# Kernel tuning notes

Measured on AMD Instinct MI355X. Metric: run time of the kernel, lower is better.

The kernel has to match this reference:

```python
import jax, jax.numpy as jnp
import numpy as np

N = 100000      # nodes
E = 1600000     # edges (before self loops)
M = 40          # n_markers
HID = 128       # hidden
HEADS = 4
DH = HID // HEADS  # 32 per-head dim
LAT = 64
NEG_SLOPE = 0.2
EPS = 1e-5


def setup_inputs() -> dict:
    key = jax.random.key(0)
    ks = jax.random.split(key, 20)
    r = lambda k, shape, s=0.05: (jax.random.normal(k, shape, jnp.float32) * s)
    x = jax.random.normal(ks[0], (N, M), jnp.float32)
    edge_index = jax.random.randint(ks[1], (2, E), 0, N, jnp.int64)
    return {
        "x": x,
        "edge_index": edge_index,
        "Wp": r(ks[2], (M, HID)), "bp": jnp.zeros((HID,), jnp.float32),
        "W1l": r(ks[3], (HID, HID)), "W1r": r(ks[4], (HID, HID)),
        "att1": r(ks[5], (HEADS, DH)), "b1": jnp.zeros((HID,), jnp.float32),
        "W2l": r(ks[6], (HID, HID)), "W2r": r(ks[7], (HID, HID)),
        "att2": r(ks[8], (HEADS, DH)), "b2": jnp.zeros((HID,), jnp.float32),
        "g1": jnp.ones((HID,), jnp.float32), "be1": jnp.zeros((HID,), jnp.float32),
        "g2": jnp.ones((HID,), jnp.float32), "be2": jnp.zeros((HID,), jnp.float32),
        "Wo": r(ks[9], (HID, LAT)), "bo": jnp.zeros((LAT,), jnp.float32),
    }


def _layernorm(z, g, b):
    mu = jnp.mean(z, axis=-1, keepdims=True)
    var = jnp.mean(jnp.square(z - mu), axis=-1, keepdims=True)
    return (z - mu) * jax.lax.rsqrt(var + EPS) * g + b


def _gatv2(h, src, dst, Wl, Wr, att, bias):
    # h: [N, HID]; per-head source/target projections (GATv2, share_weights=False)
    hl = (h @ Wl).reshape(N, HEADS, DH)  # messages (source side)
    hr = (h @ Wr).reshape(N, HEADS, DH)  # target side
    # per-edge attention logits: a^T LeakyReLU(hl[src] + hr[dst])
    e = jax.nn.leaky_relu(hl[src] + hr[dst], NEG_SLOPE)      # [Etot, HEADS, DH]
    logits = jnp.einsum('ehd,hd->eh', e, att)                # [Etot, HEADS]
    # segment softmax over edges sharing the same destination node
    m = jax.ops.segment_max(logits, dst, num_segments=N)     # [N, HEADS]
    ex = jnp.exp(logits - m[dst])
    denom = jax.ops.segment_sum(ex, dst, num_segments=N)     # [N, HEADS]
    alpha = ex / denom[dst]                                  # [Etot, HEADS]
    # scatter-aggregate weighted source messages
    out = jax.ops.segment_sum(hl[src] * alpha[:, :, None], dst, num_segments=N)
    return out.reshape(N, HID) + bias


def reference(x, edge_index, Wp, bp, W1l, W1r, att1, b1, W2l, W2r, att2, b2,
              g1, be1, g2, be2, Wo, bo):
    loops = jnp.arange(N, dtype=edge_index.dtype)
    src = jnp.concatenate([edge_index[0], loops])  # PyG adds self loops by default
    dst = jnp.concatenate([edge_index[1], loops])
    h = x @ Wp + bp
    h = _layernorm(jax.nn.gelu(_gatv2(h, src, dst, W1l, W1r, att1, b1), approximate=False) + h, g1, be1)
    h = _layernorm(jax.nn.gelu(_gatv2(h, src, dst, W2l, W2r, att2, b2), approximate=False) + h, g2, be2)
    return h @ Wo + bo
```

## Files before the change

### kernel.cpp

```cpp
#include <hip/hip_runtime.h>
#include <hip/hip_bf16.h>
#include <math.h>

#define NN   100000
#define EE   1600000
#define ETOT 1700000
#define MM   40
#define HID  128
#define LAT  64
#define NB   391
#define CHUNK 4096

typedef unsigned short u16;
typedef unsigned int   u32;
typedef unsigned long long u64;

typedef __attribute__((ext_vector_type(8))) short bf16x8;
typedef __attribute__((ext_vector_type(4))) float f32x4;
typedef __attribute__((ext_vector_type(2))) float f32x2;

__device__ __forceinline__ float bf2f(u16 a) {
    return __uint_as_float(((u32)a) << 16);
}
__device__ __forceinline__ u16 f2bf(float f) {
    u32 u = __float_as_uint(f);
    u32 r = (u + 0x7fffu + ((u >> 16) & 1u)) >> 16;
    return (u16)r;
}
__device__ __forceinline__ f32x2 unpk(u32 u) {
    f32x2 r;
    r.x = __uint_as_float(u << 16);
    r.y = __uint_as_float(u & 0xffff0000u);
    return r;
}
__device__ __forceinline__ float exp2_hw(float x) {
    float d;
    asm("v_exp_f32 %0, %1" : "=v"(d) : "v"(x));
    return d;
}
__device__ __forceinline__ void gload_lds16(const void* g, void* l) {
    __builtin_amdgcn_global_load_lds(
        (const __attribute__((address_space(1))) void*)g,
        (__attribute__((address_space(3))) void*)l, 16, 0, 0);
}
__device__ __forceinline__ float gelu_t(float x) {
    float x2 = x * x;
    float y = x * fmaf(0.0713548162726f, x2, 1.59576912161f);
    return x / (1.f + __expf(-y));
}

#define Vbp   0
#define Vatt1 128
#define Vb1   256
#define Vg1   384
#define Vbe1  512
#define Vatt2 640
#define Vb2   768
#define Vg2   896
#define Vbe2  1024
#define Vbo   1152
#define VTOT  1216

#define BWp   0
#define BW1l  8192
#define BW1r  24576
#define BW2l  40960
#define BW2r  57344
#define BWo   73728
#define BTOT  90112

#define NXB   15625
#define NVB   5
#define NWB   352

__device__ __forceinline__ int sniff_bf_wave(const u32* __restrict__ x_raw) {
    int lane = threadIdx.x & 63;
    u32 w = x_raw[lane];
    u16 lo = (u16)(w & 0xffffu);
    int e = (lo >> 7) & 0xFF;
    int ok = (e >= 118 && e <= 133) ? 1 : 0;
    u64 b = __ballot(ok);
    return (__popcll(b) >= 48) ? 1 : 0;
}

__device__ __forceinline__ void edge_decode(const int* __restrict__ ei, int is64, int e,
                                            int& src, int& dst) {
    if (e < EE) {
        src = is64 ? ei[2 * e] : ei[e];
        int idx = EE + e;
        dst = is64 ? ei[2 * idx] : ei[idx];
    } else {
        src = e - EE; dst = src;
    }
}

__global__ __launch_bounds__(256) void prep_kernel(
    const void* __restrict__ x, const u32* __restrict__ ei_raw,
    const void* p0, const void* p1, const void* p2, const void* p3, const void* p4,
    const void* p5, const void* p6, const void* p7, const void* p8, const void* p9,
    const void* w0, const void* w1, const void* w2, const void* w3, const void* w4,
    const void* w5,
    u16* __restrict__ xb, float* __restrict__ wv, u16* __restrict__ wbf,
    int* __restrict__ flags, u32* __restrict__ gbucket, u32* __restrict__ dcnt,
    u32* __restrict__ gcur, u32* __restrict__ dcur)
{
    const u32* x_raw = (const u32*)x;
    int isbf = sniff_bf_wave(x_raw);
    int t = threadIdx.x;
    int b = blockIdx.x;

    if (b == 0) {
        if (t < 64) {
            u32 a = ei_raw[2 * t + 1] | ei_raw[129 + 2 * t];
            u64 nz = __ballot(a != 0u);
            if (t == 0) { flags[0] = (nz == 0uLL) ? 1 : 0; flags[1] = isbf; }
        }
        gbucket[t] = 0; gbucket[t + 256] = 0;
        gcur[t] = 0;    gcur[t + 256] = 0;
        if (t < 64) { dcnt[t] = 0; dcur[t] = 0; }
        return;
    }
    if (b <= NXB) {
        int i = (b - 1) * 256 + t;
        xb[i] = isbf ? ((const u16*)x)[i] : f2bf(((const float*)x)[i]);
        return;
    }
    if (b <= NXB + NVB) {
        int i = (b - 1 - NXB) * 256 + t;
        if (i >= VTOT) return;
        const int offs[11] = {Vbp, Vatt1, Vb1, Vg1, Vbe1, Vatt2, Vb2, Vg2, Vbe2, Vbo, VTOT};
        const void* ps[10] = {p0,p1,p2,p3,p4,p5,p6,p7,p8,p9};
        int s = 0;
#pragma unroll
        for (int k = 1; k < 10; k++) s += (i >= offs[k]) ? 1 : 0;
        int j = i - offs[s];
        const void* p = ps[s];
        wv[i] = isbf ? bf2f(((const u16*)p)[j]) : ((const float*)p)[j];
        return;
    }
    {
        int i = (b - 1 - NXB - NVB) * 256 + t;
        const int offs[7] = {BWp, BW1l, BW1r, BW2l, BW2r, BWo, BTOT};
        const int Ks[6]   = {40, 128, 128, 128, 128, 128};
        const int Ncs[6]  = {128, 128, 128, 128, 128, 64};
        const int Kps[6]  = {64, 128, 128, 128, 128, 128};
        const void* ps[6] = {w0,w1,w2,w3,w4,w5};
        int s = 0;
#pragma unroll
        for (int k = 1; k < 6; k++) s += (i >= offs[k]) ? 1 : 0;
        int j = i - offs[s];
        int Kp = Kps[s];
        int n = j / Kp, k = j % Kp;
        u16 v = 0;
        if (k < Ks[s] && n < Ncs[s]) {
            const void* p = ps[s];
            int src = k * Ncs[s] + n;
            v = isbf ? ((const u16*)p)[src] : f2bf(((const float*)p)[src]);
        }
        wbf[i] = v;
    }
}

__global__ __launch_bounds__(256) void bucket_hist_kernel(
    const int* __restrict__ ei, const int* __restrict__ flags, u32* __restrict__ gbucket)
{
    __shared__ u32 h[512];
    int t = threadIdx.x;
    h[t] = 0; h[t + 256] = 0;
    __syncthreads();
    int is64 = flags[0];
    int base = blockIdx.x * CHUNK;
#pragma unroll
    for (int j = 0; j < CHUNK / 256; j++) {
        int e = base + j * 256 + t;
        if (e < ETOT) {
            int src, dst;
            edge_decode(ei, is64, e, src, dst);
            atomicAdd(&h[dst >> 8], 1u);
        }
    }
    __syncthreads();
    if (h[t])       atomicAdd(&gbucket[t], h[t]);
    if (h[t + 256]) atomicAdd(&gbucket[t + 256], h[t + 256]);
}

__global__ __launch_bounds__(256) void bin_pass_kernel(
    const int* __restrict__ ei, const int* __restrict__ flags,
    const u32* __restrict__ gbucket, u32* __restrict__ gcur, u64* __restrict__ pairs)
{
    __shared__ u32 bh[512];
    __shared__ u32 boff[512];
    __shared__ u32 bbs[512];
    __shared__ u32 bcur[512];
    __shared__ u32 bsc[512];
    __shared__ u64 stage[CHUNK];
    __shared__ u32 ts[256];

    int t = threadIdx.x;
    bh[t] = 0; bh[t + 256] = 0;
    __syncthreads();
    int is64 = flags[0];
    int base = blockIdx.x * CHUNK;
    int chunk_n = ETOT - base; if (chunk_n > CHUNK) chunk_n = CHUNK;

#pragma unroll
    for (int j = 0; j < CHUNK / 256; j++) {
        int e = base + j * 256 + t;
        if (e < ETOT) {
            int src, dst;
            edge_decode(ei, is64, e, src, dst);
            atomicAdd(&bh[dst >> 8], 1u);
        }
    }
    __syncthreads();

    {
        u32 g0v = (2 * t     < NB) ? gbucket[2 * t]     : 0;
        u32 g1v = (2 * t + 1 < NB) ? gbucket[2 * t + 1] : 0;
        u32 ps = g0v + g1v;
        ts[t] = ps; __syncthreads();
        for (int d = 1; d < 256; d <<= 1) {
            u32 v = (t >= d) ? ts[t - d] : 0;
            __syncthreads();
            ts[t] += v;
            __syncthreads();
        }
        u32 ex = ts[t] - ps;
        bsc[2 * t] = ex; bsc[2 * t + 1] = ex + g0v;
    }
    __syncthreads();

    u32 s0 = bh[2 * t], s1 = bh[2 * t + 1];
    u32 tsum = s0 + s1;
    ts[t] = tsum; __syncthreads();
    for (int d = 1; d < 256; d <<= 1) {
        u32 v = (t >= d) ? ts[t - d] : 0;
        __syncthreads();
        ts[t] += v;
        __syncthreads();
    }
    u32 excl = ts[t] - tsum;
    boff[2 * t] = excl; boff[2 * t + 1] = excl + s0;
    bcur[2 * t] = excl; bcur[2 * t + 1] = excl + s0;
    __syncthreads();
    if (t < NB && bh[t]) bbs[t] = bsc[t] + atomicAdd(&gcur[t], bh[t]);
    if (t + 256 < NB && bh[t + 256]) bbs[t + 256] = bsc[t + 256] + atomicAdd(&gcur[t + 256], bh[t + 256]);
    __syncthreads();
#pragma unroll
    for (int j = 0; j < CHUNK / 256; j++) {
        int e = base + j * 256 + t;
        if (e < ETOT) {
            int src, dst;
            edge_decode(ei, is64, e, src, dst);
            u32 pos = atomicAdd(&bcur[dst >> 8], 1u);
            stage[pos] = (u64)src | ((u64)dst << 32);
        }
    }
    __syncthreads();
    for (int i = t; i < chunk_n; i += 256) {
        u64 pr = stage[i];
        u32 b = (u32)(pr >> 32) >> 8;
        pairs[(size_t)bbs[b] + (i - boff[b])] = pr;
    }
}

__global__ __launch_bounds__(256) void sort_pass_kernel(
    const u64* __restrict__ pairs, const u32* __restrict__ gbucket,
    int* __restrict__ srcs, int* __restrict__ offs, u32* __restrict__ dcnt)
{
    __shared__ u32 nh[256];
    __shared__ u32 ns[256];
    __shared__ u32 ncur[256];
    __shared__ u32 dh[64];
    __shared__ u32 bsc[512];
    int t = threadIdx.x;
    int b = blockIdx.x;

    {
        u32 g0v = (2 * t     < NB) ? gbucket[2 * t]     : 0;
        u32 g1v = (2 * t + 1 < NB) ? gbucket[2 * t + 1] : 0;
        u32 ps = g0v + g1v;
        ns[t] = ps; __syncthreads();
        for (int d = 1; d < 256; d <<= 1) {
            u32 v = (t >= d) ? ns[t - d] : 0;
            __syncthreads();
            ns[t] += v;
            __syncthreads();
        }
        u32 ex = ns[t] - ps;
        bsc[2 * t] = ex; bsc[2 * t + 1] = ex + g0v;
    }
    __syncthreads();
    u32 beg = bsc[b], endp = bsc[b + 1];

    nh[t] = 0;
    if (t < 64) dh[t] = 0;
    __syncthreads();
    for (u32 i = beg + t; i < endp; i += 256) {
        u32 dst = (u32)(pairs[i] >> 32);
        atomicAdd(&nh[dst & 255], 1u);
    }
    __syncthreads();
    u32 cnt = nh[t];
    ns[t] = cnt; __syncthreads();
    for (int d = 1; d < 256; d <<= 1) {
        u32 v = (t >= d) ? ns[t - d] : 0;
        __syncthreads();
        ns[t] += v;
        __syncthreads();
    }
    u32 excl = ns[t] - cnt;
    int id = b * 256 + t;
    if (id <= NN) offs[id] = (int)(beg + excl);
    if (id < NN) atomicAdd(&dh[cnt < 63u ? cnt : 63u], 1u);
    ncur[t] = excl;
    __syncthreads();
    if (t < 64 && dh[t]) atomicAdd(&dcnt[t], dh[t]);
    for (u32 i = beg + t; i < endp; i += 256) {
        u64 pr = pairs[i];
        u32 loc = ((u32)(pr >> 32)) & 255;
        u32 p = atomicAdd(&ncur[loc], 1u);
        srcs[beg + p] = (int)(u32)pr;
    }
}

__global__ __launch_bounds__(256) void deg_perm_kernel(
    const int* __restrict__ offs, const u32* __restrict__ dcnt,
    u32* __restrict__ dcur, int* __restrict__ perm)
{
    __shared__ u32 cnt[64];
    __shared__ u32 base[64];
    __shared__ u32 sb[64];
    int t = threadIdx.x;
    if (t < 64) {
        u32 v = dcnt[t];
        u32 x = v;
#pragma unroll
        for (int off = 1; off < 64; off <<= 1) {
            u32 y = __shfl_down(x, off);
            if (t + off < 64) x += y;
        }
        sb[t] = x - v;
        cnt[t] = 0;
    }
    __syncthreads();
    int i = blockIdx.x * 256 + t;
    int d = 0; u32 r = 0;
    bool ok = (i < NN);
    if (ok) {
        d = offs[i + 1] - offs[i];
        if (d > 63) d = 63;
        r = atomicAdd(&cnt[d], 1u);
    }
    __syncthreads();
    if (t < 64 && cnt[t]) base[t] = sb[t] + atomicAdd(&dcur[t], cnt[t]);
    __syncthreads();
    if (ok) perm[base[d] + r] = i;
}

__global__ __launch_bounds__(256) void mfma_gemm(
    const u16* __restrict__ A, int lda,
    const u16* __restrict__ Bt, int ldb,
    const float* __restrict__ bias,
    int nrows, int ksteps, int ncols,
    float* __restrict__ outF, u16* __restrict__ outB, u16* __restrict__ outB2, int ldo,
    int mode, const int* __restrict__ flags)
{
    int lane = threadIdx.x & 63;
    int wv = threadIdx.x >> 6;
    int wx = wv & 1, wy = wv >> 1;
    int l16 = lane & 15, quad = lane >> 4;
    int r0 = blockIdx.x * 128 + wx * 64;
    int n0 = wy * 64;

    Bt += (size_t)blockIdx.y * 128 * ldb;
    if (blockIdx.y) outB = outB2;

    f32x4 acc[4][4];
#pragma unroll
    for (int m = 0; m < 4; m++)
#pragma unroll
        for (int n = 0; n < 4; n++) acc[m][n] = (f32x4){0.f, 0.f, 0.f, 0.f};

    const u16* Ap = A + (size_t)(r0 + l16) * lda + quad * 8;
    const u16* Bp = Bt + (size_t)(n0 + l16) * ldb + quad * 8;

    for (int k = 0; k < ksteps; ++k) {
        bf16x8 af[4], bfr[4];
#pragma unroll
        for (int m = 0; m < 4; m++)
            af[m] = *(const bf16x8*)(Ap + (size_t)m * 16 * lda + k * 32);
#pragma unroll
        for (int n = 0; n < 4; n++)
            bfr[n] = *(const bf16x8*)(Bp + (size_t)n * 16 * ldb + k * 32);
#pragma unroll
        for (int m = 0; m < 4; m++)
#pragma unroll
            for (int n = 0; n < 4; n++)
                acc[m][n] = __builtin_amdgcn_mfma_f32_16x16x32_bf16(af[m], bfr[n], acc[m][n], 0, 0, 0);
    }

    int mk = mode;
    if (mk < 0) mk = flags[1] ? 2 : 1;

#pragma unroll
    for (int m = 0; m < 4; m++) {
#pragma unroll
        for (int n = 0; n < 4; n++) {
            int col = n0 + n * 16 + l16;
            float bb = (bias != nullptr && col < ncols) ? bias[col] : 0.f;
#pragma unroll
            for (int reg = 0; reg < 4; reg++) {
                int row = r0 + m * 16 + quad * 4 + reg;
                if (row < nrows && col < ncols) {
                    float v = acc[m][n][reg] + bb;
                    if (mk & 1) outF[(size_t)row * ldo + col] = v;
                    if (mk & 2) outB[(size_t)row * ldo + col] = f2bf(v);
                }
            }
        }
    }
}

__global__ __launch_bounds__(256) void gemm_layer(
    const u16* __restrict__ A,
    const u16* __restrict__ Bt,
    u16* __restrict__ outL, u16* __restrict__ outR)
{
    __shared__ u16 Atile[64 * 128];
    int t = threadIdx.x;
    int wv = t >> 6, lane = t & 63;
    int l16 = lane & 15, quad = lane >> 4;
    int r0 = blockIdx.x * 64;

    {
        const char* Ab = (const char*)(A + (size_t)r0 * 128);
        char* Lb = (char*)Atile + wv * 4096;
        u32 baseP = (u32)(wv * 4096) + (u32)lane * 16;
#pragma unroll
        for (int j = 0; j < 4; j++) {
            u32 P = baseP + (u32)(j * 1024);
            u32 row = P >> 8;
            u32 L = P ^ ((row & 7u) << 4);
            gload_lds16(Ab + L, Lb + j * 1024);
        }
    }

    f32x4 acc[4][4];
#pragma unroll
    for (int m = 0; m < 4; m++)
#pragma unroll
        for (int n = 0; n < 4; n++) acc[m][n] = (f32x4){0.f, 0.f, 0.f, 0.f};

    int n0 = wv * 64;
    const u16* Bp = Bt + (size_t)(n0 + l16) * 128 + quad * 8;
    const char* At = (const char*)Atile;

    __syncthreads();

#pragma unroll
    for (int k = 0; k < 4; k++) {
        bf16x8 af[4], bfr[4];
#pragma unroll
        for (int n = 0; n < 4; n++)
            bfr[n] = *(const bf16x8*)(Bp + (size_t)n * 16 * 128 + k * 32);
#pragma unroll
        for (int m = 0; m < 4; m++) {
            u32 arow = (u32)(m * 16 + l16);
            u32 Lb = arow * 256 + (u32)(quad * 16 + k * 64);
            u32 Pb = Lb ^ ((arow & 7u) << 4);
            af[m] = *(const bf16x8*)(At + Pb);
        }
#pragma unroll
        for (int m = 0; m < 4; m++)
#pragma unroll
            for (int n = 0; n < 4; n++)
                acc[m][n] = __builtin_amdgcn_mfma_f32_16x16x32_bf16(af[m], bfr[n], acc[m][n], 0, 0, 0);
    }

    u16* outp = (wv < 2) ? outL : outR;
    int nb = n0 & 127;
#pragma unroll
    for (int m = 0; m < 4; m++) {
#pragma unroll
        for (int n = 0; n < 4; n++) {
            int col = nb + n * 16 + l16;
#pragma unroll
            for (int reg = 0; reg < 4; reg++) {
                int row = r0 + m * 16 + quad * 4 + reg;
                if (row < NN)
                    outp[(size_t)row * 128 + col] = f2bf(acc[m][n][reg]);
            }
        }
    }
}

__global__ __launch_bounds__(256) void gat_agg_kernel(
    const u16* __restrict__ hl, const u16* __restrict__ hr, const u16* __restrict__ hresb,
    const float* __restrict__ att, const float* __restrict__ bias,
    const float* __restrict__ gamma, const float* __restrict__ beta,
    const int* __restrict__ offs, const int* __restrict__ srcs,
    const int* __restrict__ perm,
    u16* __restrict__ outb)
{
    int lane = threadIdx.x & 63;
    int sub = lane >> 4;
    int r = lane & 15;
    int c0 = r * 8;
    u32 cb = (u32)(r << 4);
    int id = (blockIdx.x * 4 + (threadIdx.x >> 6)) * 4 + sub;
    int dst = perm[id];

    int start = offs[dst];
    int deg = offs[dst + 1] - start;
    int dm = deg - 1;
    const char* hlc = (const char*)hl;

    f32x2 hr2[4], av2[4];
    {
        uint4 q = *(const uint4*)((const char*)hr + ((u32)dst << 8) + cb);
        hr2[0] = unpk(q.x); hr2[1] = unpk(q.y); hr2[2] = unpk(q.z); hr2[3] = unpk(q.w);
        const float L2E = 1.4426950408889634f;
        float4 a0 = *(const float4*)&att[c0];
        float4 a1 = *(const float4*)&att[c0 + 4];
        av2[0] = (f32x2){L2E * a0.x, L2E * a0.y}; av2[1] = (f32x2){L2E * a0.z, L2E * a0.w};
        av2[2] = (f32x2){L2E * a1.x, L2E * a1.y}; av2[3] = (f32x2){L2E * a1.z, L2E * a1.w};
    }

    int md = deg;
    md = max(md, __shfl_xor(md, 16));
    md = max(md, __shfl_xor(md, 32));

    f32x2 acc2[4];
#pragma unroll
    for (int i = 0; i < 4; i++) acc2[i] = (f32x2){0.f, 0.f};
    float s = 0.f;

    int sa = srcs[start];
    int sb = srcs[start + (1 < dm ? 1 : dm)];
    uint4 qa = *(const uint4*)(hlc + ((u32)sa << 8) + cb);
    uint4 qb = *(const uint4*)(hlc + ((u32)sb << 8) + cb);
    int sna = srcs[start + (2 < dm ? 2 : dm)];
    int snb = srcs[start + (3 < dm ? 3 : dm)];

    int mi = (md + 1) >> 1;
    for (int j = 0; j < mi; ++j) {
        int e4 = 2 * j + 4, e5 = 2 * j + 5;
        int sna2 = srcs[start + min(e4, dm)];
        int snb2 = srcs[start + min(e5, dm)];
        uint4 qna = *(const uint4*)(hlc + ((u32)sna << 8) + cb);
        uint4 qnb = *(const uint4*)(hlc + ((u32)snb << 8) + cb);

        f32x2 ha[4], hb[4];
        ha[0] = unpk(qa.x); ha[1] = unpk(qa.y); ha[2] = unpk(qa.z); ha[3] = unpk(qa.w);
        hb[0] = unpk(qb.x); hb[1] = unpk(qb.y); hb[2] = unpk(qb.z); hb[3] = unpk(qb.w);
        f32x2 pa2 = (f32x2){0.f, 0.f};
        f32x2 pb2 = (f32x2){0.f, 0.f};
#pragma unroll
        for (int i = 0; i < 4; i++) {
            f32x2 za = ha[i] + hr2[i];
            f32x2 zb = hb[i] + hr2[i];
            f32x2 la = __builtin_elementwise_max(za, za * 0.2f);
            f32x2 lb = __builtin_elementwise_max(zb, zb * 0.2f);
            pa2 = __builtin_elementwise_fma(av2[i], la, pa2);
            pb2 = __builtin_elementwise_fma(av2[i], lb, pb2);
        }
        float pa = pa2.x + pa2.y;
        float pb = pb2.x + pb2.y;
        pa += __shfl_xor(pa, 1); pb += __shfl_xor(pb, 1);
        pa += __shfl_xor(pa, 2); pb += __shfl_xor(pb, 2);
        int e0 = 2 * j, e1 = 2 * j + 1;
        float wa = (e0 < deg) ? exp2_hw(pa) : 0.f;
        float wb = (e1 < deg) ? exp2_hw(pb) : 0.f;
        s += wa + wb;
        f32x2 wa2 = (f32x2){wa, wa};
        f32x2 wb2 = (f32x2){wb, wb};
#pragma unroll
        for (int i = 0; i < 4; i++)
            acc2[i] = __builtin_elementwise_fma(wa2, ha[i],
                      __builtin_elementwise_fma(wb2, hb[i], acc2[i]));

        qa = qna; qb = qnb; sna = sna2; snb = snb2;
    }

    float inv = 1.f / s;
    float v[8];
    {
        float4 b0 = *(const float4*)&bias[c0];
        float4 b1 = *(const float4*)&bias[c0 + 4];
        float bb[8] = {b0.x,b0.y,b0.z,b0.w,b1.x,b1.y,b1.z,b1.w};
        uint4 qr = *(const uint4*)((const char*)hresb + ((u32)dst << 8) + cb);
        f32x2 rr2[4] = {unpk(qr.x), unpk(qr.y), unpk(qr.z), unpk(qr.w)};
#pragma unroll
        for (int i = 0; i < 4; i++) {
            float t0 = fmaf(acc2[i].x, inv, bb[2*i]);
            float t1 = fmaf(acc2[i].y, inv, bb[2*i+1]);
            v[2*i]   = gelu_t(t0) + rr2[i].x;
            v[2*i+1] = gelu_t(t1) + rr2[i].y;
        }
    }

    float s1 = 0.f, s2 = 0.f;
#pragma unroll
    for (int k = 0; k < 8; k++) { s1 += v[k]; s2 = fmaf(v[k], v[k], s2); }
#pragma unroll
    for (int off = 1; off < 16; off <<= 1) {
        s1 += __shfl_xor(s1, off);
        s2 += __shfl_xor(s2, off);
    }
    float mu  = s1 * (1.f / 128.f);
    float var = s2 * (1.f / 128.f) - mu * mu;
    float rstd = rsqrtf(var + 1e-5f);

    float4 g0 = *(const float4*)&gamma[c0];
    float4 g1 = *(const float4*)&gamma[c0 + 4];
    float4 be0 = *(const float4*)&beta[c0];
    float4 be1 = *(const float4*)&beta[c0 + 4];
    float gg[8] = {g0.x,g0.y,g0.z,g0.w,g1.x,g1.y,g1.z,g1.w};
    float eb[8] = {be0.x,be0.y,be0.z,be0.w,be1.x,be1.y,be1.z,be1.w};
    float o[8];
#pragma unroll
    for (int k = 0; k < 8; k++) o[k] = fmaf((v[k] - mu) * rstd, gg[k], eb[k]);
    uint4 pk;
    pk.x = (u32)f2bf(o[0]) | ((u32)f2bf(o[1]) << 16);
    pk.y = (u32)f2bf(o[2]) | ((u32)f2bf(o[3]) << 16);
    pk.z = (u32)f2bf(o[4]) | ((u32)f2bf(o[5]) << 16);
    pk.w = (u32)f2bf(o[6]) | ((u32)f2bf(o[7]) << 16);
    *(uint4*)((char*)outb + ((u32)dst << 8) + cb) = pk;
}

extern "C" void kernel_launch(void* const* d_in, const int* in_sizes, int n_in,
                              void* d_out, int out_size, void* d_ws, size_t ws_size,
                              hipStream_t stream) {
    const void* x  = d_in[0];
    const int*  ei = (const int*)d_in[1];

    char* ws = (char*)d_ws;
    size_t off = 0;
    auto alloc = [&](size_t bytes) -> void* {
        void* p = ws + off;
        off = (off + bytes + 511) & ~(size_t)511;
        return p;
    };
    u16*   xb      = (u16*)  alloc(((size_t)NN * MM + 8192) * 2);
    float* wv      = (float*)alloc((size_t)VTOT * 4);
    u16*   wbf     = (u16*)  alloc((size_t)BTOT * 2);
    u16*   h0b     = (u16*)  alloc((size_t)(NN + 64) * HID * 2);
    u16*   h1b     = (u16*)  alloc((size_t)(NN + 64) * HID * 2);
    u16*   hlb     = (u16*)  alloc((size_t)(NN + 64) * HID * 2);
    u16*   hrb     = (u16*)  alloc((size_t)(NN + 64) * HID * 2);
    int*   offs    = (int*)  alloc((size_t)(NN + 1) * 4);
    u32*   gbucket = (u32*)  alloc(512 * 4);
    u32*   gcur    = (u32*)  alloc(512 * 4);
    int*   flags   = (int*)  alloc(512);
    int*   srcs    = (int*)  alloc(((size_t)ETOT + 64) * 4);
    u64*   pairs   = (u64*)  alloc((size_t)ETOT * 8);
    u32*   dcnt    = (u32*)  alloc(64 * 4);
    u32*   dcur    = (u32*)  alloc(64 * 4);
    int*   perm    = (int*)  alloc((size_t)NN * 4);

    prep_kernel<<<1 + NXB + NVB + NWB, 256, 0, stream>>>(
        x, (const u32*)ei,
        d_in[3], d_in[6], d_in[7], d_in[12], d_in[13], d_in[10], d_in[11], d_in[14], d_in[15], d_in[17],
        d_in[2], d_in[4], d_in[5], d_in[8], d_in[9], d_in[16],
        xb, wv, wbf, flags, gbucket, dcnt, gcur, dcur);

    const int EB = (ETOT + CHUNK - 1) / CHUNK;
    bucket_hist_kernel<<<EB, 256, 0, stream>>>(ei, flags, gbucket);
    bin_pass_kernel<<<EB, 256, 0, stream>>>(ei, flags, gbucket, gcur, pairs);
    sort_pass_kernel<<<NB, 256, 0, stream>>>(pairs, gbucket, srcs, offs, dcnt);

    deg_perm_kernel<<<NB, 256, 0, stream>>>(offs, dcnt, dcur, perm);

    const int GB = (NN + 127) / 128;
    const int LB = (NN + 63) / 64;
    const int AB = NN / 16;

    mfma_gemm<<<dim3(GB, 1), 256, 0, stream>>>(xb, MM, wbf + BWp, 64, wv + Vbp,
                                               NN, 2, HID, nullptr, h0b, nullptr, HID, 2, flags);

    gemm_layer<<<LB, 256, 0, stream>>>(h0b, wbf + BW1l, hlb, hrb);
    gat_agg_kernel<<<AB, 256, 0, stream>>>(hlb, hrb, h0b, wv + Vatt1, wv + Vb1,
                                           wv + Vg1, wv + Vbe1, offs, srcs, perm, h1b);

    gemm_layer<<<LB, 256, 0, stream>>>(h1b, wbf + BW2l, hlb, hrb);
    gat_agg_kernel<<<AB, 256, 0, stream>>>(hlb, hrb, h1b, wv + Vatt2, wv + Vb2,
                                           wv + Vg2, wv + Vbe2, offs, srcs, perm, h0b);

    mfma_gemm<<<dim3(GB, 1), 256, 0, stream>>>(h0b, HID, wbf + BWo, HID, wv + Vbo,
                                               NN, 4, LAT, (float*)d_out, (u16*)d_out, nullptr, LAT, -1, flags);
}
```

Baseline: 419.2 us.

## Pad input to 64 columns, stage GEMM A tiles in swizzled LDS, cache edges

The input conversion now writes x into a zero-padded 64-column bf16 buffer, so the projection GEMM reads aligned rows. The generic mfma_gemm is replaced by two specialised kernels, gemm_proj and gemm_final. Each loads its 128-row A tile into LDS with direct global-to-LDS copies and an XOR swizzle, and the final GEMM uses only the 64 output columns it needs instead of wasting half its waves. The bin pass keeps each decoded edge pair in registers between its histogram and scatter phases instead of decoding the edge list twice. The cost is more LDS and register use, plus a larger padded x buffer to write.

```diff
diff --git a/kernel.cpp b/kernel.cpp
--- a/kernel.cpp
+++ b/kernel.cpp
@@ -69,7 +69,8 @@
 #define BWo   73728
 #define BTOT  90112
 
-#define NXB   15625
+#define XROWS 100096
+#define NXB   25000
 #define NVB   5
 #define NWB   352
 
@@ -122,7 +123,13 @@
     }
     if (b <= NXB) {
         int i = (b - 1) * 256 + t;
-        xb[i] = isbf ? ((const u16*)x)[i] : f2bf(((const float*)x)[i]);
+        int row = i >> 6, k = i & 63;
+        u16 v = 0;
+        if (k < MM) {
+            int src = row * MM + k;
+            v = isbf ? ((const u16*)x)[src] : f2bf(((const float*)x)[src]);
+        }
+        xb[i] = v;
         return;
     }
     if (b <= NXB + NVB) {
@@ -203,12 +210,14 @@
     int base = blockIdx.x * CHUNK;
     int chunk_n = ETOT - base; if (chunk_n > CHUNK) chunk_n = CHUNK;
 
+    u64 epk[CHUNK / 256];
 #pragma unroll
     for (int j = 0; j < CHUNK / 256; j++) {
         int e = base + j * 256 + t;
         if (e < ETOT) {
             int src, dst;
             edge_decode(ei, is64, e, src, dst);
+            epk[j] = (u64)(u32)src | ((u64)(u32)dst << 32);
             atomicAdd(&bh[dst >> 8], 1u);
         }
     }
@@ -250,10 +259,9 @@
     for (int j = 0; j < CHUNK / 256; j++) {
         int e = base + j * 256 + t;
         if (e < ETOT) {
-            int src, dst;
-            edge_decode(ei, is64, e, src, dst);
-            u32 pos = atomicAdd(&bcur[dst >> 8], 1u);
-            stage[pos] = (u64)src | ((u64)dst << 32);
+            u64 pr = epk[j];
+            u32 pos = atomicAdd(&bcur[(u32)(pr >> 32) >> 8], 1u);
+            stage[pos] = pr;
         }
     }
     __syncthreads();
@@ -358,41 +366,57 @@
     if (ok) perm[base[d] + r] = i;
 }
 
-__global__ __launch_bounds__(256) void mfma_gemm(
-    const u16* __restrict__ A, int lda,
-    const u16* __restrict__ Bt, int ldb,
+__global__ __launch_bounds__(256) void gemm_proj(
+    const u16* __restrict__ A,
+    const u16* __restrict__ Bt,
     const float* __restrict__ bias,
-    int nrows, int ksteps, int ncols,
-    float* __restrict__ outF, u16* __restrict__ outB, u16* __restrict__ outB2, int ldo,
-    int mode, const int* __restrict__ flags)
-{
-    int lane = threadIdx.x & 63;
-    int wv = threadIdx.x >> 6;
+    u16* __restrict__ outB)
+{
+    __shared__ u16 Atile[128 * 64];
+    int t = threadIdx.x;
+    int wv = t >> 6, lane = t & 63;
     int wx = wv & 1, wy = wv >> 1;
     int l16 = lane & 15, quad = lane >> 4;
-    int r0 = blockIdx.x * 128 + wx * 64;
+    int r0 = blockIdx.x * 128;
+
+    {
+        const char* Ab = (const char*)(A + (size_t)r0 * 64);
+        char* Lb = (char*)Atile + wv * 4096;
+        u32 baseP = (u32)(wv * 4096) + (u32)lane * 16;
+#pragma unroll
+        for (int j = 0; j < 4; j++) {
+            u32 P = baseP + (u32)(j * 1024);
+            u32 row = P >> 7;
+            u32 L = P ^ ((row & 7u) << 4);
+            gload_lds16(Ab + L, Lb + j * 1024);
+        }
+    }
+
+    f32x4 acc[4][4];
+#pragma unroll
+    for (int m = 0; m < 4; m++)
+#pragma unroll
+        for (int n = 0; n < 4; n++) acc[m][n] = (f32x4){0.f, 0.f, 0.f, 0.f};
+
     int n0 = wy * 64;
-
-    Bt += (size_t)blockIdx.y * 128 * ldb;
-    if (blockIdx.y) outB = outB2;
-
-    f32x4 acc[4][4];
-#pragma unroll
-    for (int m = 0; m < 4; m++)
-#pragma unroll
-        for (int n = 0; n < 4; n++) acc[m][n] = (f32x4){0.f, 0.f, 0.f, 0.f};
-
-    const u16* Ap = A + (size_t)(r0 + l16) * lda + quad * 8;
-    const u16* Bp = Bt + (size_t)(n0 + l16) * ldb + quad * 8;
-
-    for (int k = 0; k < ksteps; ++k) {
+    const u16* Bp = Bt + (size_t)(n0 + l16) * 64 + quad * 8;
+    const char* At = (const char*)Atile;
+
+    __syncthreads();
+
+#pragma unroll
+    for (int k = 0; k < 2; k++) {
         bf16x8 af[4], bfr[4];
 #pragma unroll
-        for (int m = 0; m < 4; m++)
-            af[m] = *(const bf16x8*)(Ap + (size_t)m * 16 * lda + k * 32);
-#pragma unroll
         for (int n = 0; n < 4; n++)
-            bfr[n] = *(const bf16x8*)(Bp + (size_t)n * 16 * ldb + k * 32);
+            bfr[n] = *(const bf16x8*)(Bp + (size_t)n * 16 * 64 + k * 32);
+#pragma unroll
+        for (int m = 0; m < 4; m++) {
+            u32 arow = (u32)(wx * 64 + m * 16 + l16);
+            u32 Lb = arow * 128 + (u32)(quad * 16 + k * 64);
+            u32 Pb = Lb ^ ((arow & 7u) << 4);
+            af[m] = *(const bf16x8*)(At + Pb);
+        }
 #pragma unroll
         for (int m = 0; m < 4; m++)
 #pragma unroll
@@ -400,23 +424,17 @@
                 acc[m][n] = __builtin_amdgcn_mfma_f32_16x16x32_bf16(af[m], bfr[n], acc[m][n], 0, 0, 0);
     }
 
-    int mk = mode;
-    if (mk < 0) mk = flags[1] ? 2 : 1;
-
 #pragma unroll
     for (int m = 0; m < 4; m++) {
 #pragma unroll
         for (int n = 0; n < 4; n++) {
             int col = n0 + n * 16 + l16;
-            float bb = (bias != nullptr && col < ncols) ? bias[col] : 0.f;
+            float bb = bias[col];
 #pragma unroll
             for (int reg = 0; reg < 4; reg++) {
-                int row = r0 + m * 16 + quad * 4 + reg;
-                if (row < nrows && col < ncols) {
-                    float v = acc[m][n][reg] + bb;
-                    if (mk & 1) outF[(size_t)row * ldo + col] = v;
-                    if (mk & 2) outB[(size_t)row * ldo + col] = f2bf(v);
-                }
+                int row = r0 + wx * 64 + m * 16 + quad * 4 + reg;
+                if (row < NN)
+                    outB[(size_t)row * 128 + col] = f2bf(acc[m][n][reg] + bb);
             }
         }
     }
@@ -490,6 +508,85 @@
                 int row = r0 + m * 16 + quad * 4 + reg;
                 if (row < NN)
                     outp[(size_t)row * 128 + col] = f2bf(acc[m][n][reg]);
+            }
+        }
+    }
+}
+
+__global__ __launch_bounds__(256) void gemm_final(
+    const u16* __restrict__ A,
+    const u16* __restrict__ Bt,
+    const float* __restrict__ bias,
+    float* __restrict__ outF, u16* __restrict__ outB,
+    const int* __restrict__ flags)
+{
+    __shared__ u16 Atile[128 * 128];
+    int t = threadIdx.x;
+    int wv = t >> 6, lane = t & 63;
+    int wx = wv & 1, wy = wv >> 1;
+    int l16 = lane & 15, quad = lane >> 4;
+    int r0 = blockIdx.x * 128;
+
+    {
+        const char* Ab = (const char*)(A + (size_t)r0 * 128);
+        char* Lb = (char*)Atile + wv * 8192;
+        u32 baseP = (u32)(wv * 8192) + (u32)lane * 16;
+#pragma unroll
+        for (int j = 0; j < 8; j++) {
+            u32 P = baseP + (u32)(j * 1024);
+            u32 row = P >> 8;
+            u32 L = P ^ ((row & 7u) << 4);
+            gload_lds16(Ab + L, Lb + j * 1024);
+        }
+    }
+
+    f32x4 acc[4][2];
+#pragma unroll
+    for (int m = 0; m < 4; m++)
+#pragma unroll
+        for (int n = 0; n < 2; n++) acc[m][n] = (f32x4){0.f, 0.f, 0.f, 0.f};
+
+    int n0 = wy * 32;
+    const u16* Bp = Bt + (size_t)(n0 + l16) * 128 + quad * 8;
+    const char* At = (const char*)Atile;
+
+    __syncthreads();
+
+#pragma unroll
+    for (int k = 0; k < 4; k++) {
+        bf16x8 af[4], bfr[2];
+#pragma unroll
+        for (int n = 0; n < 2; n++)
+            bfr[n] = *(const bf16x8*)(Bp + (size_t)n * 16 * 128 + k * 32);
+#pragma unroll
+        for (int m = 0; m < 4; m++) {
+            u32 arow = (u32)(wx * 64 + m * 16 + l16);
+            u32 Lb = arow * 256 + (u32)(quad * 16 + k * 64);
+            u32 Pb = Lb ^ ((arow & 7u) << 4);
+            af[m] = *(const bf16x8*)(At + Pb);
+        }
+#pragma unroll
+        for (int m = 0; m < 4; m++)
+#pragma unroll
+            for (int n = 0; n < 2; n++)
+                acc[m][n] = __builtin_amdgcn_mfma_f32_16x16x32_bf16(af[m], bfr[n], acc[m][n], 0, 0, 0);
+    }
+
+    int mk = flags[1] ? 2 : 1;
+#pragma unroll
+    for (int m = 0; m < 4; m++) {
+#pragma unroll
+        for (int n = 0; n < 2; n++) {
+            int col = n0 + n * 16 + l16;
+            float bb = bias[col];
+#pragma unroll
+            for (int reg = 0; reg < 4; reg++) {
+                int row = r0 + wx * 64 + m * 16 + quad * 4 + reg;
+                if (row < NN) {
+                    float v = acc[m][n][reg] + bb;
+                    if (mk & 1) outF[(size_t)row * 64 + col] = v;
+                    if (mk & 2) outB[(size_t)row * 64 + col] = f2bf(v);
+                }
             }
         }
     }
@@ -642,13 +739,13 @@
         off = (off + bytes + 511) & ~(size_t)511;
         return p;
     };
-    u16*   xb      = (u16*)  alloc(((size_t)NN * MM + 8192) * 2);
+    u16*   xb      = (u16*)  alloc((size_t)XROWS * 64 * 2);
     float* wv      = (float*)alloc((size_t)VTOT * 4);
     u16*   wbf     = (u16*)  alloc((size_t)BTOT * 2);
-    u16*   h0b     = (u16*)  alloc((size_t)(NN + 64) * HID * 2);
-    u16*   h1b     = (u16*)  alloc((size_t)(NN + 64) * HID * 2);
-    u16*   hlb     = (u16*)  alloc((size_t)(NN + 64) * HID * 2);
-    u16*   hrb     = (u16*)  alloc((size_t)(NN + 64) * HID * 2);
+    u16*   h0b     = (u16*)  alloc((size_t)(NN + 128) * HID * 2);
+    u16*   h1b     = (u16*)  alloc((size_t)(NN + 128) * HID * 2);
+    u16*   hlb     = (u16*)  alloc((size_t)(NN + 128) * HID * 2);
+    u16*   hrb     = (u16*)  alloc((size_t)(NN + 128) * HID * 2);
     int*   offs    = (int*)  alloc((size_t)(NN + 1) * 4);
     u32*   gbucket = (u32*)  alloc(512 * 4);
     u32*   gcur    = (u32*)  alloc(512 * 4);
@@ -676,8 +773,7 @@
     const int LB = (NN + 63) / 64;
     const int AB = NN / 16;
 
-    mfma_gemm<<<dim3(GB, 1), 256, 0, stream>>>(xb, MM, wbf + BWp, 64, wv + Vbp,
-                                               NN, 2, HID, nullptr, h0b, nullptr, HID, 2, flags);
+    gemm_proj<<<GB, 256, 0, stream>>>(xb, wbf + BWp, wv + Vbp, h0b);
 
     gemm_layer<<<LB, 256, 0, stream>>>(h0b, wbf + BW1l, hlb, hrb);
     gat_agg_kernel<<<AB, 256, 0, stream>>>(hlb, hrb, h0b, wv + Vatt1, wv + Vb1,
@@ -687,6 +783,6 @@
     gat_agg_kernel<<<AB, 256, 0, stream>>>(hlb, hrb, h1b, wv + Vatt2, wv + Vb2,
                                            wv + Vg2, wv + Vbe2, offs, srcs, perm, h0b);
 
-    mfma_gemm<<<dim3(GB, 1), 256, 0, stream>>>(h0b, HID, wbf + BWo, HID, wv + Vbo,
-                                               NN, 4, LAT, (float*)d_out, (u16*)d_out, nullptr, LAT, -1, flags);
-}
+    gemm_final<<<GB, 256, 0, stream>>>(h0b, wbf + BWo, wv + Vbo,
+                                       (float*)d_out, (u16*)d_out, flags);
+}
```

Measured after the change: 401.4 us. -4.3%, faster.
